# Optimization experiments

Measured on AMD Instinct MI355X. Metric: run time of the kernel, lower is better.

Reference implementation:

```python
import jax, jax.numpy as jnp
import numpy as np

HIDDEN = 1024
EXPAND = 2
D_REC = HIDDEN * EXPAND
INTER = 4096
B, T = 4, 4096


def _rmsnorm(x, w, eps=1e-6):
    var = jnp.mean(x * x, axis=-1, keepdims=True)
    return x * jax.lax.rsqrt(var + eps) * w


def setup_inputs() -> dict:
    key = jax.random.key(0)
    ks = jax.random.split(key, 11)
    s = lambda fan: 1.0 / np.sqrt(fan)
    return {
        "x": jax.random.normal(ks[0], (B, T, HIDDEN), dtype=jnp.float32),
        "ln1_w": jnp.ones((HIDDEN,), dtype=jnp.float32),
        "ln2_w": jnp.ones((HIDDEN,), dtype=jnp.float32),
        "w_in": jax.random.normal(ks[1], (D_REC, HIDDEN), dtype=jnp.float32) * s(HIDDEN),
        "w_gate": jax.random.normal(ks[2], (D_REC, HIDDEN), dtype=jnp.float32) * s(HIDDEN),
        "a_param": jax.random.normal(ks[3], (D_REC,), dtype=jnp.float32) * 0.1,
        "w_a": jax.random.normal(ks[4], (D_REC, D_REC), dtype=jnp.float32) * s(D_REC),
        "w_out": jax.random.normal(ks[5], (HIDDEN, D_REC), dtype=jnp.float32) * s(D_REC),
        "w_mlp_gate": jax.random.normal(ks[6], (INTER, HIDDEN), dtype=jnp.float32) * s(HIDDEN),
        "w_mlp_up": jax.random.normal(ks[7], (INTER, HIDDEN), dtype=jnp.float32) * s(HIDDEN),
        "w_mlp_down": jax.random.normal(ks[8], (HIDDEN, INTER), dtype=jnp.float32) * s(INTER),
    }


def _hawk_scan(x_in, a):
    # x_in, a: [B, T, D_REC]; h_t = a_t*h_{t-1} + sqrt(1-a_t^2+eps)*x_t
    xs = jnp.moveaxis(x_in, 1, 0)  # [T, B, D]
    As = jnp.moveaxis(a, 1, 0)

    def step(state, inp):
        a_t, x_t = inp
        new = a_t * state + jnp.sqrt(1.0 - a_t * a_t + 1e-8) * x_t
        return new, new

    init = jnp.zeros(x_in.shape[::2], dtype=x_in.dtype)  # [B, D]
    _, ys = jax.lax.scan(step, init, (As, xs))
    return jnp.moveaxis(ys, 0, 1)  # [B, T, D]


def reference(x, ln1_w, ln2_w, w_in, w_gate, a_param, w_a, w_out,
              w_mlp_gate, w_mlp_up, w_mlp_down):
    h = _rmsnorm(x, ln1_w)
    x_in = h @ w_in.T                     # [B,T,D_REC]
    gate = jax.nn.sigmoid(h @ w_gate.T)
    a = jax.nn.sigmoid(a_param + x_in @ w_a.T)
    y = gate * _hawk_scan(x_in, a)
    x = x + y @ w_out.T
    h2 = _rmsnorm(x, ln2_w)
    mlp = (jax.nn.silu(h2 @ w_mlp_gate.T) * (h2 @ w_mlp_up.T)) @ w_mlp_down.T
    return x + mlp
```

## Files before the change

kernel.cpp:

```cpp
#include <hip/hip_runtime.h>
#include <cstdint>
#include <cmath>


typedef unsigned short u16;
typedef _Float16 f16;
typedef __bf16 bf16x8 __attribute__((ext_vector_type(8)));
typedef float  f32x4  __attribute__((ext_vector_type(4)));

#define BM 128
#define BN 128
#define BK 64

#define HID   1024
#define DREC  2048
#define INTER 4096
#define BT    16384
#define TLEN  4096
#define NCHAN 8192
#define CHUNK 64
#define NCH   64
#define NPAIR 4096

__device__ __forceinline__ float b2f(u16 u) {
  union { unsigned int i; float f; } v; v.i = ((unsigned int)u) << 16; return v.f;
}
__device__ __forceinline__ u16 f2bf(float f) {
  unsigned int u = __builtin_bit_cast(unsigned int, f);
  u += 0x7FFFu + ((u >> 16) & 1u);
  return (u16)(u >> 16);
}
__device__ __forceinline__ float sigm(float x) { return 1.f / (1.f + expf(-x)); }

typedef __attribute__((address_space(1))) void as1_void;
typedef __attribute__((address_space(3))) void as3_void;
__device__ __forceinline__ void async16(const void* g, void* l) {
  __builtin_amdgcn_global_load_lds((as1_void*)g, (as3_void*)l, 16, 0, 0);
}

__global__ void f2b_all(const float* s0, const float* s1, const float* s2,
                        const float* s3, const float* s4, const float* s5,
                        const float* s6,
                        u16* d0, u16* d1, u16* d2, u16* d3, u16* d4, u16* d5,
                        u16* d6) {
  int blk = blockIdx.x;
  const float* src; u16* dst; int rel;
  if      (blk < 2048)  { src = s0; dst = d0; rel = blk; }
  else if (blk < 4096)  { src = s1; dst = d1; rel = blk - 2048; }
  else if (blk < 8192)  { src = s2; dst = d2; rel = blk - 4096; }
  else if (blk < 10240) { src = s3; dst = d3; rel = blk - 8192; }
  else if (blk < 14336) { src = s4; dst = d4; rel = blk - 10240; }
  else if (blk < 18432) { src = s5; dst = d5; rel = blk - 14336; }
  else                  { src = s6; dst = d6; rel = blk - 18432; }
  int i = rel * 256 + threadIdx.x;
  float4 v = ((const float4*)src)[i];
  ushort4 o;
  o.x = f2bf(v.x); o.y = f2bf(v.y); o.z = f2bf(v.z); o.w = f2bf(v.w);
  ((ushort4*)dst)[i] = o;
}

__global__ void rmsnorm_kernel(const float* __restrict__ x, const float* __restrict__ w,
                               u16* __restrict__ out) {
  const int row = blockIdx.x;
  const int tid = threadIdx.x;
  float4 v = ((const float4*)(x + (size_t)row * HID))[tid];
  float ss = v.x * v.x + v.y * v.y + v.z * v.z + v.w * v.w;
#pragma unroll
  for (int o = 32; o > 0; o >>= 1) ss += __shfl_down(ss, o);
  __shared__ float red[4];
  const int lane = tid & 63, wv = tid >> 6;
  if (lane == 0) red[wv] = ss;
  __syncthreads();
  float tot = red[0] + red[1] + red[2] + red[3];
  float sc = rsqrtf(tot * (1.f / (float)HID) + 1e-6f);
  float4 wv4 = ((const float4*)w)[tid];
  ushort4 o;
  o.x = f2bf(v.x * sc * wv4.x); o.y = f2bf(v.y * sc * wv4.y);
  o.z = f2bf(v.z * sc * wv4.z); o.w = f2bf(v.w * sc * wv4.w);
  ((ushort4*)(out + (size_t)row * HID))[tid] = o;
}

enum { EPI_LOGIT = 0, EPI_ADDF = 1 };

template <int EPI>
__global__ __launch_bounds__(256, 3)
void gemm1(const u16* __restrict__ A, const u16* __restrict__ W,
           int K, int N, int ldA, int ldW,
           float* outf, f16* outz, const float* auxf) {
  __shared__ alignas(16) u16 sA[BM * BK];
  __shared__ alignas(16) u16 sB[BN * BK];

  const int tid  = threadIdx.x;
  const int lane = tid & 63;
  const int wv   = tid >> 6;
  const int wm   = wv & 1;
  const int wn   = wv >> 1;
  const int lm   = lane & 15;
  const int quad = lane >> 4;

  const int row0 = blockIdx.x * BM;
  const int col0 = blockIdx.y * BN;

  f32x4 acc[4][4];
#pragma unroll
  for (int i = 0; i < 4; ++i)
#pragma unroll
    for (int j = 0; j < 4; ++j) acc[i][j] = (f32x4)0.f;

  for (int k0 = 0; k0 < K; k0 += BK) {
#pragma unroll
    for (int i = 0; i < 4; ++i) {
      int p = i * 256 + tid;
      int r = p >> 3;
      int sg = (p & 7) ^ (r & 7);
      async16(A + (size_t)(row0 + r) * ldA + (k0 + sg * 8), (char*)sA + p * 16);
    }
#pragma unroll
    for (int i = 0; i < 4; ++i) {
      int p = i * 256 + tid;
      int r = p >> 3;
      int sg = (p & 7) ^ (r & 7);
      async16(W + (size_t)(col0 + r) * ldW + (k0 + sg * 8), (char*)sB + p * 16);
    }
    __syncthreads();

#pragma unroll
    for (int h = 0; h < 2; ++h) {
      bf16x8 af[4], bf[4];
#pragma unroll
      for (int mi = 0; mi < 4; ++mi) {
        int r = wm * 64 + mi * 16 + lm;
        af[mi] = ((const bf16x8*)sA)[r * 8 + ((h * 4 + quad) ^ (r & 7))];
      }
#pragma unroll
      for (int ni = 0; ni < 4; ++ni) {
        int c = wn * 64 + ni * 16 + lm;
        bf[ni] = ((const bf16x8*)sB)[c * 8 + ((h * 4 + quad) ^ (c & 7))];
      }
#pragma unroll
      for (int mi = 0; mi < 4; ++mi)
#pragma unroll
        for (int ni = 0; ni < 4; ++ni)
          acc[mi][ni] = __builtin_amdgcn_mfma_f32_16x16x32_bf16(af[mi], bf[ni], acc[mi][ni], 0, 0, 0);
    }
    __syncthreads();
  }

#pragma unroll
  for (int mi = 0; mi < 4; ++mi) {
    const int rbase = row0 + wm * 64 + mi * 16 + quad * 4;
#pragma unroll
    for (int ni = 0; ni < 4; ++ni) {
      const int cg = col0 + wn * 64 + ni * 16 + lm;
      f32x4 v = acc[mi][ni];
#pragma unroll
      for (int rr = 0; rr < 4; ++rr) {
        size_t idx = (size_t)(rbase + rr) * N + cg;
        float t = v[rr];
        if constexpr (EPI == EPI_LOGIT) {
          outz[idx] = (f16)(t + auxf[cg]);
        } else {
          outf[idx] = t + auxf[idx];
        }
      }
    }
  }
}

enum { EPI2_XG = 0, EPI2_SM = 1 };

template <int EPI>
__global__ __launch_bounds__(256, 3)
void gemm2(const u16* __restrict__ A, const u16* __restrict__ W0,
           const u16* __restrict__ W1,
           int K, int N, int ldA, int ldW,
           u16* out0, u16* out1) {
  __shared__ alignas(16) u16 sA[BM * BK];
  __shared__ alignas(16) u16 sB0[64 * BK];
  __shared__ alignas(16) u16 sB1[64 * BK];

  const int tid  = threadIdx.x;
  const int lane = tid & 63;
  const int wv   = tid >> 6;
  const int wm   = wv & 1;
  const int wn   = wv >> 1;
  const int lm   = lane & 15;
  const int quad = lane >> 4;

  const int row0 = blockIdx.x * BM;
  const int col0 = blockIdx.y * 64;

  f32x4 acc0[4][2], acc1[4][2];
#pragma unroll
  for (int i = 0; i < 4; ++i)
#pragma unroll
    for (int j = 0; j < 2; ++j) { acc0[i][j] = (f32x4)0.f; acc1[i][j] = (f32x4)0.f; }

  for (int k0 = 0; k0 < K; k0 += BK) {
#pragma unroll
    for (int i = 0; i < 4; ++i) {
      int p = i * 256 + tid;
      int r = p >> 3;
      int sg = (p & 7) ^ (r & 7);
      async16(A + (size_t)(row0 + r) * ldA + (k0 + sg * 8), (char*)sA + p * 16);
    }
#pragma unroll
    for (int i = 0; i < 2; ++i) {
      int p = i * 256 + tid;
      int r = p >> 3;
      int sg = (p & 7) ^ (r & 7);
      size_t go = (size_t)(col0 + r) * ldW + (k0 + sg * 8);
      async16(W0 + go, (char*)sB0 + p * 16);
      async16(W1 + go, (char*)sB1 + p * 16);
    }
    __syncthreads();

#pragma unroll
    for (int h = 0; h < 2; ++h) {
      bf16x8 af[4], b0[2], b1[2];
#pragma unroll
      for (int mi = 0; mi < 4; ++mi) {
        int r = wm * 64 + mi * 16 + lm;
        af[mi] = ((const bf16x8*)sA)[r * 8 + ((h * 4 + quad) ^ (r & 7))];
      }
#pragma unroll
      for (int ni = 0; ni < 2; ++ni) {
        int c = wn * 32 + ni * 16 + lm;
        int o = c * 8 + ((h * 4 + quad) ^ (c & 7));
        b0[ni] = ((const bf16x8*)sB0)[o];
        b1[ni] = ((const bf16x8*)sB1)[o];
      }
#pragma unroll
      for (int mi = 0; mi < 4; ++mi)
#pragma unroll
        for (int ni = 0; ni < 2; ++ni) {
          acc0[mi][ni] = __builtin_amdgcn_mfma_f32_16x16x32_bf16(af[mi], b0[ni], acc0[mi][ni], 0, 0, 0);
          acc1[mi][ni] = __builtin_amdgcn_mfma_f32_16x16x32_bf16(af[mi], b1[ni], acc1[mi][ni], 0, 0, 0);
        }
    }
    __syncthreads();
  }

#pragma unroll
  for (int mi = 0; mi < 4; ++mi) {
    const int rbase = row0 + wm * 64 + mi * 16 + quad * 4;
#pragma unroll
    for (int ni = 0; ni < 2; ++ni) {
      const int cg = col0 + wn * 32 + ni * 16 + lm;
#pragma unroll
      for (int rr = 0; rr < 4; ++rr) {
        size_t idx = (size_t)(rbase + rr) * N + cg;
        float v0 = acc0[mi][ni][rr];
        float v1 = acc1[mi][ni][rr];
        if constexpr (EPI == EPI2_XG) {
          out0[idx] = f2bf(v0);
          out1[idx] = f2bf(sigm(v1));
        } else {
          out0[idx] = f2bf(v0 * sigm(v0) * v1);
        }
      }
    }
  }
}

__global__ void scan_phase1(const f16* __restrict__ z, const u16* __restrict__ xin,
                            float2* __restrict__ ch_h, float2* __restrict__ ch_p) {
  int gtid = blockIdx.x * 256 + threadIdx.x;
  int c = gtid >> 12;
  int pair = gtid & (NPAIR - 1);
  int b = pair >> 10;
  int d = (pair & 1023) * 2;
  size_t base = ((size_t)b * TLEN + (size_t)c * CHUNK) * DREC + d;
  float2 h = {0.f, 0.f}, P = {1.f, 1.f};
#pragma unroll 8
  for (int t = 0; t < CHUNK; ++t) {
    size_t i = base + (size_t)t * DREC;
    f16 z2[2]; *(uint32_t*)z2 = *(const uint32_t*)(z + i);
    u16 x2[2]; *(uint32_t*)x2 = *(const uint32_t*)(xin + i);
    float a0 = sigm((float)z2[0]), a1 = sigm((float)z2[1]);
    h.x = a0 * h.x + sqrtf(1.f - a0 * a0 + 1e-8f) * b2f(x2[0]);
    h.y = a1 * h.y + sqrtf(1.f - a1 * a1 + 1e-8f) * b2f(x2[1]);
    P.x *= a0; P.y *= a1;
  }
  ch_h[gtid] = h;
  ch_p[gtid] = P;
}

__global__ void scan_phase2(float2* __restrict__ ch_h, const float2* __restrict__ ch_p) {
  int pair = blockIdx.x * 256 + threadIdx.x;
  float2 H = {0.f, 0.f};
#pragma unroll
  for (int c = 0; c < NCH; ++c) {
    int i = c * NPAIR + pair;
    float2 he = ch_h[i];
    float2 P  = ch_p[i];
    ch_h[i] = H;
    H.x = he.x + P.x * H.x;
    H.y = he.y + P.y * H.y;
  }
}

__global__ void scan_phase3(const f16* __restrict__ z, const u16* __restrict__ xin,
                            u16* gate_y, const float2* __restrict__ ch_h) {
  int gtid = blockIdx.x * 256 + threadIdx.x;
  int c = gtid >> 12;
  int pair = gtid & (NPAIR - 1);
  int b = pair >> 10;
  int d = (pair & 1023) * 2;
  size_t base = ((size_t)b * TLEN + (size_t)c * CHUNK) * DREC + d;
  float2 h = ch_h[gtid];
#pragma unroll 8
  for (int t = 0; t < CHUNK; ++t) {
    size_t i = base + (size_t)t * DREC;
    f16 z2[2]; *(uint32_t*)z2 = *(const uint32_t*)(z + i);
    u16 x2[2]; *(uint32_t*)x2 = *(const uint32_t*)(xin + i);
    u16 g2[2]; *(uint32_t*)g2 = *(const uint32_t*)(gate_y + i);
    float a0 = sigm((float)z2[0]), a1 = sigm((float)z2[1]);
    h.x = a0 * h.x + sqrtf(1.f - a0 * a0 + 1e-8f) * b2f(x2[0]);
    h.y = a1 * h.y + sqrtf(1.f - a1 * a1 + 1e-8f) * b2f(x2[1]);
    u16 o2[2];
    o2[0] = f2bf(b2f(g2[0]) * h.x);
    o2[1] = f2bf(b2f(g2[1]) * h.y);
    *(uint32_t*)(gate_y + i) = *(uint32_t*)o2;
  }
}

extern "C" void kernel_launch(void* const* d_in, const int* in_sizes, int n_in,
                              void* d_out, int out_size, void* d_ws, size_t ws_size,
                              hipStream_t stream) {
  const float* x      = (const float*)d_in[0];
  const float* ln1    = (const float*)d_in[1];
  const float* ln2    = (const float*)d_in[2];
  const float* w_in   = (const float*)d_in[3];
  const float* w_gate = (const float*)d_in[4];
  const float* a_par  = (const float*)d_in[5];
  const float* w_a    = (const float*)d_in[6];
  const float* w_out  = (const float*)d_in[7];
  const float* w_mg   = (const float*)d_in[8];
  const float* w_mu   = (const float*)d_in[9];
  const float* w_md   = (const float*)d_in[10];
  float* out = (float*)d_out;
  char* ws = (char*)d_ws;

  const size_t MB = 1024ull * 1024ull;
  u16* wb_in  = (u16*)(ws + 0 * MB);
  u16* wb_gt  = (u16*)(ws + 4 * MB);
  u16* wb_a   = (u16*)(ws + 8 * MB);
  u16* wb_out = (u16*)(ws + 16 * MB);
  u16* wb_mg  = (u16*)(ws + 20 * MB);
  u16* wb_mu  = (u16*)(ws + 28 * MB);
  u16* wb_md  = (u16*)(ws + 36 * MB);
  u16* hbuf  = (u16*)(ws + 44 * MB);
  f16* zbuf  = (f16*)(ws + 44 * MB);
  u16* gateb = (u16*)(ws + 108 * MB);
  u16* mbuf  = (u16*)(ws + 108 * MB);
  float2* chh = (float2*)(ws + 0 * MB);
  float2* chp = (float2*)(ws + 2 * MB);
  u16* xinb = (u16*)d_out;

  f2b_all<<<22528, 256, 0, stream>>>(w_in, w_gate, w_a, w_out, w_mg, w_mu, w_md,
                                     wb_in, wb_gt, wb_a, wb_out, wb_mg, wb_mu, wb_md);

  rmsnorm_kernel<<<BT, 256, 0, stream>>>(x, ln1, hbuf);

  gemm2<EPI2_XG><<<dim3(BT / BM, DREC / 64), 256, 0, stream>>>(
      hbuf, wb_in, wb_gt, HID, DREC, HID, HID, xinb, gateb);

  gemm1<EPI_LOGIT><<<dim3(BT / BM, DREC / BN), 256, 0, stream>>>(
      xinb, wb_a, DREC, DREC, DREC, DREC, nullptr, zbuf, a_par);

  scan_phase1<<<NCH * NPAIR / 256, 256, 0, stream>>>(zbuf, xinb, chh, chp);
  scan_phase2<<<NPAIR / 256, 256, 0, stream>>>(chh, chp);
  scan_phase3<<<NCH * NPAIR / 256, 256, 0, stream>>>(zbuf, xinb, gateb, chh);

  gemm1<EPI_ADDF><<<dim3(BT / BM, HID / BN), 256, 0, stream>>>(
      gateb, wb_out, DREC, HID, DREC, DREC, out, nullptr, x);

  rmsnorm_kernel<<<BT, 256, 0, stream>>>(out, ln2, hbuf);

  for (int half = 0; half < 2; ++half) {
    const u16* wmg_h = wb_mg + (size_t)half * 2048 * HID;
    const u16* wmu_h = wb_mu + (size_t)half * 2048 * HID;
    const u16* wmd_h = wb_md + (size_t)half * 2048;
    gemm2<EPI2_SM><<<dim3(BT / BM, 2048 / 64), 256, 0, stream>>>(
        hbuf, wmg_h, wmu_h, HID, 2048, HID, HID, mbuf, nullptr);
    gemm1<EPI_ADDF><<<dim3(BT / BM, HID / BN), 256, 0, stream>>>(
        mbuf, wmd_h, 2048, HID, 2048, INTER, out, nullptr, out);
  }
}
```

Before: 1.195 ms.

## Replace GEMMs with 256x256 double-buffered 8-wave pipelined kernels

```diff
diff --git a/kernel.cpp b/kernel.cpp
--- a/kernel.cpp
+++ b/kernel.cpp
@@ -7,10 +7,6 @@
 typedef _Float16 f16;
 typedef __bf16 bf16x8 __attribute__((ext_vector_type(8)));
 typedef float  f32x4  __attribute__((ext_vector_type(4)));
-
-#define BM 128
-#define BN 128
-#define BK 64
 
 #define HID   1024
 #define DREC  2048
@@ -37,6 +33,11 @@
 __device__ __forceinline__ void async16(const void* g, void* l) {
   __builtin_amdgcn_global_load_lds((as1_void*)g, (as3_void*)l, 16, 0, 0);
 }
+
+#define BARSYNC() do { __builtin_amdgcn_s_barrier(); __builtin_amdgcn_sched_barrier(0); } while (0)
+#define LGKM0()   do { asm volatile("s_waitcnt lgkmcnt(0)" ::: "memory"); __builtin_amdgcn_sched_barrier(0); } while (0)
+#define VMC(N)    do { asm volatile("s_waitcnt vmcnt(" #N ")" ::: "memory"); __builtin_amdgcn_sched_barrier(0); } while (0)
+#define FENCE()   do { asm volatile("" ::: "memory"); __builtin_amdgcn_sched_barrier(0); } while (0)
 
 __global__ void f2b_all(const float* s0, const float* s1, const float* s2,
                         const float* s3, const float* s4, const float* s5,
@@ -80,87 +81,137 @@
   ((ushort4*)(out + (size_t)row * HID))[tid] = o;
 }
 
+__device__ __forceinline__ void stageG(const u16* __restrict__ g, int ldg,
+                                       int rb, int k0, u16* lbase, int tid) {
+#pragma unroll
+  for (int i = 0; i < 2; ++i) {
+    int p = i * 512 + tid;
+    int r = p >> 3;
+    int sg = (p & 7) ^ (r & 7);
+    async16(g + (size_t)(rb + r) * ldg + (k0 + sg * 8), (char*)lbase + p * 16);
+  }
+}
+
+__device__ __forceinline__ void readA4(bf16x8 (&af)[4][2], const u16* base,
+                                       int rbase, int quad) {
+#pragma unroll
+  for (int i = 0; i < 4; ++i) {
+    int r = rbase + i * 16;
+#pragma unroll
+    for (int ks = 0; ks < 2; ++ks)
+      af[i][ks] = ((const bf16x8*)base)[r * 8 + ((ks * 4 + quad) ^ (r & 7))];
+  }
+}
+__device__ __forceinline__ void readB2(bf16x8 (&bf)[2][2], const u16* base,
+                                       int rbase, int quad) {
+#pragma unroll
+  for (int i = 0; i < 2; ++i) {
+    int r = rbase + i * 16;
+#pragma unroll
+    for (int ks = 0; ks < 2; ++ks)
+      bf[i][ks] = ((const bf16x8*)base)[r * 8 + ((ks * 4 + quad) ^ (r & 7))];
+  }
+}
+
+template <int MI0, int NI0, int NA>
+__device__ __forceinline__ void mfmaQ(f32x4 (&acc)[8][NA],
+                                      const bf16x8 (&af)[4][2],
+                                      const bf16x8 (&bf)[2][2]) {
+  __builtin_amdgcn_s_setprio(1);
+#pragma unroll
+  for (int mi = 0; mi < 4; ++mi)
+#pragma unroll
+    for (int ni = 0; ni < 2; ++ni)
+#pragma unroll
+      for (int ks = 0; ks < 2; ++ks)
+        acc[MI0 + mi][NI0 + ni] = __builtin_amdgcn_mfma_f32_16x16x32_bf16(
+            af[mi][ks], bf[ni][ks], acc[MI0 + mi][NI0 + ni], 0, 0, 0);
+  __builtin_amdgcn_s_setprio(0);
+}
+
 enum { EPI_LOGIT = 0, EPI_ADDF = 1 };
 
 template <int EPI>
-__global__ __launch_bounds__(256, 3)
-void gemm1(const u16* __restrict__ A, const u16* __restrict__ W,
-           int K, int N, int ldA, int ldW,
-           float* outf, f16* outz, const float* auxf) {
-  __shared__ alignas(16) u16 sA[BM * BK];
-  __shared__ alignas(16) u16 sB[BN * BK];
-
+__global__ __launch_bounds__(512, 2)
+void gemm256(const u16* __restrict__ A, const u16* __restrict__ W,
+             int K, int N, int ldA, int ldW,
+             float* outf, f16* outz, const float* auxf) {
+  __shared__ u16 sA[2][16384];
+  __shared__ u16 sB[2][16384];
   const int tid  = threadIdx.x;
-  const int lane = tid & 63;
-  const int wv   = tid >> 6;
-  const int wm   = wv & 1;
-  const int wn   = wv >> 1;
-  const int lm   = lane & 15;
-  const int quad = lane >> 4;
-
-  const int row0 = blockIdx.x * BM;
-  const int col0 = blockIdx.y * BN;
-
-  f32x4 acc[4][4];
-#pragma unroll
-  for (int i = 0; i < 4; ++i)
+  const int lane = tid & 63, wv = tid >> 6;
+  const int wm   = wv >> 2, wn = wv & 3;
+  const int lm   = lane & 15, quad = lane >> 4;
+  const int row0 = blockIdx.x * 256, col0 = blockIdx.y * 256;
+  const int NT   = K >> 6;
+
+  f32x4 acc[8][4];
+#pragma unroll
+  for (int i = 0; i < 8; ++i)
 #pragma unroll
     for (int j = 0; j < 4; ++j) acc[i][j] = (f32x4)0.f;
 
-  for (int k0 = 0; k0 < K; k0 += BK) {
-#pragma unroll
-    for (int i = 0; i < 4; ++i) {
-      int p = i * 256 + tid;
-      int r = p >> 3;
-      int sg = (p & 7) ^ (r & 7);
-      async16(A + (size_t)(row0 + r) * ldA + (k0 + sg * 8), (char*)sA + p * 16);
+  stageG(A, ldA, row0,       0, sA[0],        tid);
+  stageG(W, ldW, col0,       0, sB[0],        tid);
+  stageG(A, ldA, row0 + 128, 0, sA[0] + 8192, tid);
+  stageG(W, ldW, col0 + 128, 0, sB[0] + 8192, tid);
+  FENCE();
+  if (NT > 1) {
+    stageG(W, ldW, col0, 64, sB[1], tid);
+    stageG(A, ldA, row0, 64, sA[1], tid);
+    VMC(4);
+  } else {
+    VMC(0);
+  }
+  BARSYNC();
+
+  for (int t = 0; t < NT; ++t) {
+    const int b = t & 1;
+    const u16* Ab = sA[b];
+    const u16* Bb = sB[b];
+    bf16x8 af[4][2], bfL[2][2], bfH[2][2];
+
+    readA4(af, Ab, wm * 128 + lm, quad);
+    readB2(bfL, Bb, wn * 64 + lm, quad);
+    if (t + 1 < NT) {
+      stageG(A, ldA, row0 + 128, (t + 1) * 64, sA[b ^ 1] + 8192, tid);
+      stageG(W, ldW, col0 + 128, (t + 1) * 64, sB[b ^ 1] + 8192, tid);
     }
-#pragma unroll
-    for (int i = 0; i < 4; ++i) {
-      int p = i * 256 + tid;
-      int r = p >> 3;
-      int sg = (p & 7) ^ (r & 7);
-      async16(W + (size_t)(col0 + r) * ldW + (k0 + sg * 8), (char*)sB + p * 16);
-    }
-    __syncthreads();
-
-#pragma unroll
-    for (int h = 0; h < 2; ++h) {
-      bf16x8 af[4], bf[4];
-#pragma unroll
-      for (int mi = 0; mi < 4; ++mi) {
-        int r = wm * 64 + mi * 16 + lm;
-        af[mi] = ((const bf16x8*)sA)[r * 8 + ((h * 4 + quad) ^ (r & 7))];
-      }
-#pragma unroll
-      for (int ni = 0; ni < 4; ++ni) {
-        int c = wn * 64 + ni * 16 + lm;
-        bf[ni] = ((const bf16x8*)sB)[c * 8 + ((h * 4 + quad) ^ (c & 7))];
-      }
-#pragma unroll
-      for (int mi = 0; mi < 4; ++mi)
-#pragma unroll
-        for (int ni = 0; ni < 4; ++ni)
-          acc[mi][ni] = __builtin_amdgcn_mfma_f32_16x16x32_bf16(af[mi], bf[ni], acc[mi][ni], 0, 0, 0);
-    }
-    __syncthreads();
-  }
-
-#pragma unroll
-  for (int mi = 0; mi < 4; ++mi) {
-    const int rbase = row0 + wm * 64 + mi * 16 + quad * 4;
+    BARSYNC(); LGKM0();
+    mfmaQ<0, 0>(acc, af, bfL);
+    BARSYNC();
+
+    readB2(bfH, Bb, wn * 64 + 32 + lm, quad);
+    BARSYNC(); LGKM0();
+    mfmaQ<0, 2>(acc, af, bfH);
+    BARSYNC();
+
+    readA4(af, Ab, wm * 128 + 64 + lm, quad);
+    if (t + 2 < NT) stageG(W, ldW, col0, (t + 2) * 64, sB[b], tid);
+    BARSYNC(); LGKM0();
+    mfmaQ<4, 2>(acc, af, bfH);
+    BARSYNC();
+
+    if (t + 2 < NT) stageG(A, ldA, row0, (t + 2) * 64, sA[b], tid);
+    mfmaQ<4, 0>(acc, af, bfL);
+    if (t + 2 < NT) { VMC(4); } else { VMC(0); }
+    BARSYNC();
+  }
+
+#pragma unroll
+  for (int mi = 0; mi < 8; ++mi) {
+    const int rb = row0 + wm * 128 + mi * 16 + quad * 4;
 #pragma unroll
     for (int ni = 0; ni < 4; ++ni) {
       const int cg = col0 + wn * 64 + ni * 16 + lm;
       f32x4 v = acc[mi][ni];
 #pragma unroll
       for (int rr = 0; rr < 4; ++rr) {
-        size_t idx = (size_t)(rbase + rr) * N + cg;
-        float t = v[rr];
+        size_t idx = (size_t)(rb + rr) * N + cg;
         if constexpr (EPI == EPI_LOGIT) {
-          outz[idx] = (f16)(t + auxf[cg]);
+          outz[idx] = (f16)(v[rr] + auxf[cg]);
         } else {
-          outf[idx] = t + auxf[idx];
+          outf[idx] = v[rr] + auxf[idx];
         }
       }
     }
@@ -170,86 +221,82 @@
 enum { EPI2_XG = 0, EPI2_SM = 1 };
 
 template <int EPI>
-__global__ __launch_bounds__(256, 3)
-void gemm2(const u16* __restrict__ A, const u16* __restrict__ W0,
-           const u16* __restrict__ W1,
-           int K, int N, int ldA, int ldW,
-           u16* out0, u16* out1) {
-  __shared__ alignas(16) u16 sA[BM * BK];
-  __shared__ alignas(16) u16 sB0[64 * BK];
-  __shared__ alignas(16) u16 sB1[64 * BK];
-
+__global__ __launch_bounds__(512, 2)
+void gemm256d(const u16* __restrict__ A, const u16* __restrict__ W0,
+              const u16* __restrict__ W1,
+              int K, int N, int ldA, int ldW,
+              u16* out0, u16* out1) {
+  __shared__ u16 sA[2][16384];
+  __shared__ u16 sB[2][16384];
   const int tid  = threadIdx.x;
-  const int lane = tid & 63;
-  const int wv   = tid >> 6;
-  const int wm   = wv & 1;
-  const int wn   = wv >> 1;
-  const int lm   = lane & 15;
-  const int quad = lane >> 4;
-
-  const int row0 = blockIdx.x * BM;
-  const int col0 = blockIdx.y * 64;
-
-  f32x4 acc0[4][2], acc1[4][2];
-#pragma unroll
-  for (int i = 0; i < 4; ++i)
+  const int lane = tid & 63, wv = tid >> 6;
+  const int wm   = wv >> 2, wn = wv & 3;
+  const int lm   = lane & 15, quad = lane >> 4;
+  const int row0 = blockIdx.x * 256, col0 = blockIdx.y * 128;
+  const int NT   = K >> 6;
+
+  f32x4 acc0[8][2], acc1[8][2];
+#pragma unroll
+  for (int i = 0; i < 8; ++i)
 #pragma unroll
     for (int j = 0; j < 2; ++j) { acc0[i][j] = (f32x4)0.f; acc1[i][j] = (f32x4)0.f; }
 
-  for (int k0 = 0; k0 < K; k0 += BK) {
-#pragma unroll
-    for (int i = 0; i < 4; ++i) {
-      int p = i * 256 + tid;
-      int r = p >> 3;
-      int sg = (p & 7) ^ (r & 7);
-      async16(A + (size_t)(row0 + r) * ldA + (k0 + sg * 8), (char*)sA + p * 16);
+  stageG(A,  ldA, row0,       0, sA[0],        tid);
+  stageG(W0, ldW, col0,       0, sB[0],        tid);
+  stageG(A,  ldA, row0 + 128, 0, sA[0] + 8192, tid);
+  stageG(W1, ldW, col0,       0, sB[0] + 8192, tid);
+  FENCE();
+  if (NT > 1) {
+    stageG(W0, ldW, col0, 64, sB[1], tid);
+    stageG(A,  ldA, row0, 64, sA[1], tid);
+    VMC(4);
+  } else {
+    VMC(0);
+  }
+  BARSYNC();
+
+  for (int t = 0; t < NT; ++t) {
+    const int b = t & 1;
+    const u16* Ab = sA[b];
+    const u16* Bb = sB[b];
+    bf16x8 af[4][2], bf0[2][2], bf1[2][2];
+
+    readA4(af, Ab, wm * 128 + lm, quad);
+    readB2(bf0, Bb, wn * 32 + lm, quad);
+    if (t + 1 < NT) {
+      stageG(A,  ldA, row0 + 128, (t + 1) * 64, sA[b ^ 1] + 8192, tid);
+      stageG(W1, ldW, col0,       (t + 1) * 64, sB[b ^ 1] + 8192, tid);
     }
-#pragma unroll
-    for (int i = 0; i < 2; ++i) {
-      int p = i * 256 + tid;
-      int r = p >> 3;
-      int sg = (p & 7) ^ (r & 7);
-      size_t go = (size_t)(col0 + r) * ldW + (k0 + sg * 8);
-      async16(W0 + go, (char*)sB0 + p * 16);
-      async16(W1 + go, (char*)sB1 + p * 16);
-    }
-    __syncthreads();
-
-#pragma unroll
-    for (int h = 0; h < 2; ++h) {
-      bf16x8 af[4], b0[2], b1[2];
-#pragma unroll
-      for (int mi = 0; mi < 4; ++mi) {
-        int r = wm * 64 + mi * 16 + lm;
-        af[mi] = ((const bf16x8*)sA)[r * 8 + ((h * 4 + quad) ^ (r & 7))];
-      }
-#pragma unroll
-      for (int ni = 0; ni < 2; ++ni) {
-        int c = wn * 32 + ni * 16 + lm;
-        int o = c * 8 + ((h * 4 + quad) ^ (c & 7));
-        b0[ni] = ((const bf16x8*)sB0)[o];
-        b1[ni] = ((const bf16x8*)sB1)[o];
-      }
-#pragma unroll
-      for (int mi = 0; mi < 4; ++mi)
-#pragma unroll
-        for (int ni = 0; ni < 2; ++ni) {
-          acc0[mi][ni] = __builtin_amdgcn_mfma_f32_16x16x32_bf16(af[mi], b0[ni], acc0[mi][ni], 0, 0, 0);
-          acc1[mi][ni] = __builtin_amdgcn_mfma_f32_16x16x32_bf16(af[mi], b1[ni], acc1[mi][ni], 0, 0, 0);
-        }
-    }
-    __syncthreads();
-  }
-
-#pragma unroll
-  for (int mi = 0; mi < 4; ++mi) {
-    const int rbase = row0 + wm * 64 + mi * 16 + quad * 4;
+    BARSYNC(); LGKM0();
+    mfmaQ<0, 0>(acc0, af, bf0);
+    BARSYNC();
+
+    readB2(bf1, Bb + 8192, wn * 32 + lm, quad);
+    BARSYNC(); LGKM0();
+    mfmaQ<0, 0>(acc1, af, bf1);
+    BARSYNC();
+
+    readA4(af, Ab, wm * 128 + 64 + lm, quad);
+    if (t + 2 < NT) stageG(W0, ldW, col0, (t + 2) * 64, sB[b], tid);
+    BARSYNC(); LGKM0();
+    mfmaQ<4, 0>(acc1, af, bf1);
+    BARSYNC();
+
+    if (t + 2 < NT) stageG(A, ldA, row0, (t + 2) * 64, sA[b], tid);
+    mfmaQ<4, 0>(acc0, af, bf0);
+    if (t + 2 < NT) { VMC(4); } else { VMC(0); }
+    BARSYNC();
+  }
+
+#pragma unroll
+  for (int mi = 0; mi < 8; ++mi) {
+    const int rb = row0 + wm * 128 + mi * 16 + quad * 4;
 #pragma unroll
     for (int ni = 0; ni < 2; ++ni) {
       const int cg = col0 + wn * 32 + ni * 16 + lm;
 #pragma unroll
       for (int rr = 0; rr < 4; ++rr) {
-        size_t idx = (size_t)(rbase + rr) * N + cg;
+        size_t idx = (size_t)(rb + rr) * N + cg;
         float v0 = acc0[mi][ni][rr];
         float v1 = acc1[mi][ni][rr];
         if constexpr (EPI == EPI2_XG) {
@@ -363,17 +410,17 @@
 
   rmsnorm_kernel<<<BT, 256, 0, stream>>>(x, ln1, hbuf);
 
-  gemm2<EPI2_XG><<<dim3(BT / BM, DREC / 64), 256, 0, stream>>>(
+  gemm256d<EPI2_XG><<<dim3(BT / 256, DREC / 128), 512, 0, stream>>>(
       hbuf, wb_in, wb_gt, HID, DREC, HID, HID, xinb, gateb);
 
-  gemm1<EPI_LOGIT><<<dim3(BT / BM, DREC / BN), 256, 0, stream>>>(
+  gemm256<EPI_LOGIT><<<dim3(BT / 256, DREC / 256), 512, 0, stream>>>(
       xinb, wb_a, DREC, DREC, DREC, DREC, nullptr, zbuf, a_par);
 
   scan_phase1<<<NCH * NPAIR / 256, 256, 0, stream>>>(zbuf, xinb, chh, chp);
   scan_phase2<<<NPAIR / 256, 256, 0, stream>>>(chh, chp);
   scan_phase3<<<NCH * NPAIR / 256, 256, 0, stream>>>(zbuf, xinb, gateb, chh);
 
-  gemm1<EPI_ADDF><<<dim3(BT / BM, HID / BN), 256, 0, stream>>>(
+  gemm256<EPI_ADDF><<<dim3(BT / 256, HID / 256), 512, 0, stream>>>(
       gateb, wb_out, DREC, HID, DREC, DREC, out, nullptr, x);
 
   rmsnorm_kernel<<<BT, 256, 0, stream>>>(out, ln2, hbuf);
@@ -382,9 +429,9 @@
     const u16* wmg_h = wb_mg + (size_t)half * 2048 * HID;
     const u16* wmu_h = wb_mu + (size_t)half * 2048 * HID;
     const u16* wmd_h = wb_md + (size_t)half * 2048;
-    gemm2<EPI2_SM><<<dim3(BT / BM, 2048 / 64), 256, 0, stream>>>(
+    gemm256d<EPI2_SM><<<dim3(BT / 256, 2048 / 128), 512, 0, stream>>>(
         hbuf, wmg_h, wmu_h, HID, 2048, HID, HID, mbuf, nullptr);
-    gemm1<EPI_ADDF><<<dim3(BT / BM, HID / BN), 256, 0, stream>>>(
+    gemm256<EPI_ADDF><<<dim3(BT / 256, HID / 256), 512, 0, stream>>>(
         mbuf, wmd_h, 2048, HID, 2048, INTER, out, nullptr, out);
   }
 }
```

Result: slower. 1.242 ms (+3.9%).
